# Performance work log

Hardware: AMD Instinct MI355X
Metric: run time of the kernel (lower is better)

Reference implementation:

```python
import jax, jax.numpy as jnp
import numpy as np

SEQ, BZ, DIM = 2048, 16, 1024
NUM_LANG, DICT_LEN = 16, 32000


def setup_inputs() -> dict:
    key = jax.random.key(0)
    ks = jax.random.split(key, 6)
    x = jax.random.normal(ks[0], (SEQ, BZ, DIM), dtype=jnp.float32)
    # raw language ids live at the tail of the dictionary: dict_len-1-raw in [0, num_lang)
    raw = DICT_LEN - 1 - jax.random.randint(ks[1], (BZ,), 0, NUM_LANG)
    W_base = jax.random.normal(ks[2], (DIM, DIM), dtype=jnp.float32) * (DIM ** -0.5)
    b_base = jax.random.normal(ks[3], (DIM,), dtype=jnp.float32) * 0.02
    W = jax.random.uniform(ks[4], (NUM_LANG, DIM, DIM), dtype=jnp.float32) * (DIM ** -0.5)
    bias = jax.random.uniform(ks[5], (NUM_LANG, DIM), dtype=jnp.float32)
    return {"x": x, "lang_ids": raw, "W_base": W_base, "b_base": b_base,
            "W": W, "bias": bias, "dict_len": DICT_LEN, "num_lang": NUM_LANG}


def reference(x, lang_ids, W_base, b_base, W, bias, dict_len, num_lang):
    # Map raw ids to expert indices in [0, num_lang)
    ids = dict_len - 1 - lang_ids                      # [bz]
    # base_model (nn.Linear): h = x @ W_base.T + b_base
    h = jnp.einsum('sbd,ed->sbe', x, W_base) + b_base  # [seq, bz, dim]
    # The original pads each language group to max group size, runs a batched
    # einsum 'abcd,ade->abce' over languages, then scatters back with per-lang
    # bias. Mathematically each batch column j gets W[lang_j] applied:
    We = W[ids]                                        # [bz, dim, dim]
    out = jnp.einsum('sbd,bde->sbe', h, We) + bias[ids][None, :, :]
    return out
```

## Files before the change

kernel.cpp:

```cpp
#include <hip/hip_runtime.h>
#include <stdint.h>

typedef unsigned short u16;
typedef unsigned int u32;
typedef __bf16 bf16x8 __attribute__((ext_vector_type(8)));
typedef float f32x4 __attribute__((ext_vector_type(4)));

#define SEQ 2048
#define BZ 16
#define DIM 1024

__device__ __forceinline__ u16 f2bf(float f) {
    union { float f; u32 u; } a; a.f = f;
    u32 r = a.u + 0x7FFFu + ((a.u >> 16) & 1u);
    return (u16)(r >> 16);
}
__device__ __forceinline__ float bf2f(u16 u) {
    union { u32 u; float f; } a; a.u = ((u32)u) << 16;
    return a.f;
}
__device__ __forceinline__ void async16(const u16* g, u16* l) {
    __builtin_amdgcn_global_load_lds(
        (const __attribute__((address_space(1))) void*)g,
        (__attribute__((address_space(3))) void*)l, 16, 0, 0);
}

__global__ void prep_kernel(const float* __restrict__ x,
                            const float* __restrict__ W,
                            const float* __restrict__ W_base,
                            const int* __restrict__ lang_ids,
                            const int* __restrict__ dict_len,
                            u16* __restrict__ xb,
                            u16* __restrict__ Wt,
                            u16* __restrict__ Wbt)
{
    int bid = blockIdx.x;
    int t = threadIdx.x;
    if (bid < SEQ) {
        int s = bid;
        const float4* src = (const float4*)(x + (size_t)s * BZ * DIM);
        #pragma unroll
        for (int j = 0; j < 16; j++) {
            int idx = j * 256 + t;
            float4 v = src[idx];
            int e = idx * 4;
            int b = e >> 10, d = e & 1023;
            u32 lo = f2bf(v.x) | ((u32)f2bf(v.y) << 16);
            u32 hi = f2bf(v.z) | ((u32)f2bf(v.w) << 16);
            *(uint2*)(xb + ((size_t)b * SEQ + s) * DIM + d) = make_uint2(lo, hi);
        }
        return;
    }
    int tid2 = bid - SEQ;
    int z = tid2 >> 10;
    int yx = tid2 & 1023;
    int by = yx >> 5, bx = yx & 31;
    const float* S;
    u16* D;
    if (z < BZ) {
        int id = dict_len[0] - 1 - lang_ids[z];
        S = W + (size_t)id * DIM * DIM;
        D = Wbt + (size_t)z * DIM * DIM;
    } else {
        S = W_base;
        D = Wt;
    }
    __shared__ float tile[32][33];
    int tx = t & 31, ty = t >> 5;
    int x0 = bx * 32, y0 = by * 32;
    #pragma unroll
    for (int i = 0; i < 4; i++)
        tile[ty + 8 * i][tx] = S[(size_t)(y0 + ty + 8 * i) * DIM + x0 + tx];
    __syncthreads();
    #pragma unroll
    for (int i = 0; i < 4; i++)
        D[(size_t)(x0 + ty + 8 * i) * DIM + y0 + tx] = f2bf(tile[tx][ty + 8 * i]);
}

__global__ void bb_kernel(const u16* __restrict__ Wbt,
                          const float* __restrict__ b_base,
                          const float* __restrict__ bias,
                          const int* __restrict__ lang_ids,
                          const int* __restrict__ dict_len,
                          float* __restrict__ bb)
{
    int gw = blockIdx.x * 4 + (threadIdx.x >> 6);
    int b = gw >> 10;
    int f = gw & 1023;
    int lane = threadIdx.x & 63;
    const u16* row = Wbt + ((size_t)b * DIM + f) * DIM;
    float s = 0.f;
    #pragma unroll
    for (int i = 0; i < DIM / 64; i++)
        s += bf2f(row[lane + 64 * i]) * b_base[lane + 64 * i];
    #pragma unroll
    for (int off = 32; off; off >>= 1)
        s += __shfl_xor(s, off, 64);
    if (lane == 0) {
        int id = dict_len[0] - 1 - lang_ids[b];
        bb[b * DIM + f] = s + bias[(size_t)id * DIM + f];
    }
}


__global__ __launch_bounds__(256, 2)
void gemm1_kernel(const u16* __restrict__ Wbt,
                  const u16* __restrict__ Wt,
                  u16* __restrict__ CT)
{
    int bid = blockIdx.x;
    int virt = ((bid & 7) << 6) + (bid >> 3);
    int b    = virt >> 5;
    int rem  = virt & 31;
    int m0   = (rem >> 2) << 7;
    int n0   = (rem & 3) << 8;

    const u16* A = Wbt + (size_t)b * DIM * DIM;
    const u16* B = Wt;
    u16* C = CT + (size_t)b * DIM * DIM;

    __shared__ u16 As[2 * 128 * 32];
    __shared__ u16 Bs[2 * 256 * 32];

    int tid = threadIdx.x;
    int w = tid >> 6, l = tid & 63;
    int lr = l & 15, quad = l >> 4;

    int srow = l >> 2;
    int chunk = l & 3;
    const u16* gA[2]; const u16* gB[4];
    int lA[2], lB[4];
    #pragma unroll
    for (int j = 0; j < 2; j++) {
        int row = w * 32 + j * 16 + srow;
        gA[j] = A + (size_t)(m0 + row) * DIM + chunk * 8;
        lA[j] = (w * 32 + j * 16) * 32;
    }
    #pragma unroll
    for (int j = 0; j < 4; j++) {
        int row = w * 64 + j * 16 + srow;
        gB[j] = B + (size_t)(n0 + row) * DIM + chunk * 8;
        lB[j] = (w * 64 + j * 16) * 32;
    }

    f32x4 acc[8][4];
    #pragma unroll
    for (int m = 0; m < 8; m++)
        #pragma unroll
        for (int n = 0; n < 4; n++)
            #pragma unroll
            for (int e = 0; e < 4; e++) acc[m][n][e] = 0.f;

    #pragma unroll
    for (int j = 0; j < 2; j++) async16(gA[j], As + lA[j]);
    #pragma unroll
    for (int j = 0; j < 4; j++) async16(gB[j], Bs + lB[j]);
    #pragma unroll
    for (int j = 0; j < 2; j++) gA[j] += 32;
    #pragma unroll
    for (int j = 0; j < 4; j++) gB[j] += 32;
    __syncthreads();

    int cur = 0;
    for (int t = 0; t < DIM / 32; t++) {
        if (t + 1 < DIM / 32) {
            int ao = (cur ^ 1) * 4096, bo = (cur ^ 1) * 8192;
            #pragma unroll
            for (int j = 0; j < 2; j++) { async16(gA[j], As + ao + lA[j]); gA[j] += 32; }
            #pragma unroll
            for (int j = 0; j < 4; j++) { async16(gB[j], Bs + bo + lB[j]); gB[j] += 32; }
        }
        const u16* ra = As + cur * 4096;
        const u16* rb = Bs + cur * 8192;
        bf16x8 af[8], bfv[4];
        #pragma unroll
        for (int m = 0; m < 8; m++)
            af[m] = *(const bf16x8*)&ra[(m * 16 + lr) * 32 + quad * 8];
        #pragma unroll
        for (int n = 0; n < 4; n++)
            bfv[n] = *(const bf16x8*)&rb[(w * 64 + n * 16 + lr) * 32 + quad * 8];
        #pragma unroll
        for (int m = 0; m < 8; m++)
            #pragma unroll
            for (int n = 0; n < 4; n++)
                acc[m][n] = __builtin_amdgcn_mfma_f32_16x16x32_bf16(
                    af[m], bfv[n], acc[m][n], 0, 0, 0);
        __syncthreads();
        cur ^= 1;
    }
    #pragma unroll
    for (int m = 0; m < 8; m++) {
        int fr = m0 + m * 16 + quad * 4;
        #pragma unroll
        for (int n = 0; n < 4; n++) {
            int dc = n0 + w * 64 + n * 16 + lr;
            #pragma unroll
            for (int rr = 0; rr < 4; rr++)
                C[(size_t)(fr + rr) * DIM + dc] = f2bf(acc[m][n][rr]);
        }
    }
}

__global__ __launch_bounds__(256, 2)
void gemm2_kernel(const u16* __restrict__ xb,
                  const u16* __restrict__ CT,
                  const float* __restrict__ bb,
                  float* __restrict__ out)
{
    int bid = blockIdx.x;
    int virt = ((bid & 7) << 7) + (bid >> 3);
    int b    = virt >> 6;
    int rem  = virt & 63;
    int s0   = (rem >> 2) << 7;
    int f0   = (rem & 3) << 8;

    const u16* A  = xb + (size_t)b * SEQ * DIM;
    const u16* Bm = CT + (size_t)b * DIM * DIM;

    __shared__ u16 As[2 * 128 * 32];
    __shared__ u16 Bs[2 * 256 * 32];

    int tid = threadIdx.x;
    int w = tid >> 6, l = tid & 63;
    int lr = l & 15, quad = l >> 4;

    int srow = l >> 2;
    int chunk = l & 3;
    const u16* gA[2]; const u16* gB[4];
    int lA[2], lB[4];
    #pragma unroll
    for (int j = 0; j < 2; j++) {
        int row = w * 32 + j * 16 + srow;
        gA[j] = A + (size_t)(s0 + row) * DIM + chunk * 8;
        lA[j] = (w * 32 + j * 16) * 32;
    }
    #pragma unroll
    for (int j = 0; j < 4; j++) {
        int row = w * 64 + j * 16 + srow;
        gB[j] = Bm + (size_t)(f0 + row) * DIM + chunk * 8;
        lB[j] = (w * 64 + j * 16) * 32;
    }

    f32x4 acc[8][4];
    #pragma unroll
    for (int m = 0; m < 8; m++)
        #pragma unroll
        for (int n = 0; n < 4; n++)
            #pragma unroll
            for (int e = 0; e < 4; e++) acc[m][n][e] = 0.f;

    #pragma unroll
    for (int j = 0; j < 2; j++) async16(gA[j], As + lA[j]);
    #pragma unroll
    for (int j = 0; j < 4; j++) async16(gB[j], Bs + lB[j]);
    #pragma unroll
    for (int j = 0; j < 2; j++) gA[j] += 32;
    #pragma unroll
    for (int j = 0; j < 4; j++) gB[j] += 32;
    __syncthreads();

    int cur = 0;
    for (int t = 0; t < DIM / 32; t++) {
        if (t + 1 < DIM / 32) {
            int ao = (cur ^ 1) * 4096, bo = (cur ^ 1) * 8192;
            #pragma unroll
            for (int j = 0; j < 2; j++) { async16(gA[j], As + ao + lA[j]); gA[j] += 32; }
            #pragma unroll
            for (int j = 0; j < 4; j++) { async16(gB[j], Bs + bo + lB[j]); gB[j] += 32; }
        }
        const u16* ra = As + cur * 4096;
        const u16* rb = Bs + cur * 8192;
        bf16x8 af[8], bfv[4];
        #pragma unroll
        for (int m = 0; m < 8; m++)
            af[m] = *(const bf16x8*)&ra[(m * 16 + lr) * 32 + quad * 8];
        #pragma unroll
        for (int n = 0; n < 4; n++)
            bfv[n] = *(const bf16x8*)&rb[(w * 64 + n * 16 + lr) * 32 + quad * 8];
        #pragma unroll
        for (int m = 0; m < 8; m++)
            #pragma unroll
            for (int n = 0; n < 4; n++)
                acc[m][n] = __builtin_amdgcn_mfma_f32_16x16x32_bf16(
                    af[m], bfv[n], acc[m][n], 0, 0, 0);
        __syncthreads();
        cur ^= 1;
    }

    #pragma unroll
    for (int n = 0; n < 4; n++) {
        int col = f0 + w * 64 + n * 16 + lr;
        float bv = bb[b * DIM + col];
        #pragma unroll
        for (int m = 0; m < 8; m++) {
            int sr = s0 + m * 16 + quad * 4;
            #pragma unroll
            for (int rr = 0; rr < 4; rr++)
                out[((size_t)(sr + rr) * BZ + b) * DIM + col] = acc[m][n][rr] + bv;
        }
    }
}

extern "C" void kernel_launch(void* const* d_in, const int* in_sizes, int n_in,
                              void* d_out, int out_size, void* d_ws, size_t ws_size,
                              hipStream_t stream)
{
    const float* x        = (const float*)d_in[0];
    const int*   lang_ids = (const int*)d_in[1];
    const float* W_base   = (const float*)d_in[2];
    const float* b_base   = (const float*)d_in[3];
    const float* W        = (const float*)d_in[4];
    const float* bias     = (const float*)d_in[5];
    const int*   dict_len = (const int*)d_in[6];
    float* out = (float*)d_out;

    char* ws = (char*)d_ws;
    u16*  Wt  = (u16*)ws;
    u16*  Wbt = (u16*)(ws + (size_t)(2u << 20));
    u16*  CT  = (u16*)(ws + (size_t)(34u << 20));
    float* bb = (float*)(ws + (size_t)(66u << 20));
    u16*  xb  = (u16*)(ws + (size_t)(67u << 20));

    prep_kernel<<<dim3(SEQ + 17 * 1024, 1, 1), 256, 0, stream>>>(
        x, W, W_base, lang_ids, dict_len, xb, Wt, Wbt);
    bb_kernel<<<dim3(4096, 1, 1), 256, 0, stream>>>(
        Wbt, b_base, bias, lang_ids, dict_len, bb);
    gemm1_kernel<<<dim3(512, 1, 1), 256, 0, stream>>>(Wbt, Wt, CT);
    gemm2_kernel<<<dim3(1024, 1, 1), 256, 0, stream>>>(xb, CT, bb, out);
}
```

Baseline: 430.7 us.

## Dedupe per-language weight products and tighten GEMM pipeline barriers

```diff
diff --git a/kernel.cpp b/kernel.cpp
--- a/kernel.cpp
+++ b/kernel.cpp
@@ -10,6 +10,10 @@
 #define BZ 16
 #define DIM 1024
 
+#define WAIT_VM6()   asm volatile("s_waitcnt vmcnt(6)" ::: "memory")
+#define WAIT_VM0()   asm volatile("s_waitcnt vmcnt(0)" ::: "memory")
+#define MEMFENCE()   asm volatile("" ::: "memory")
+
 __device__ __forceinline__ u16 f2bf(float f) {
     union { float f; u32 u; } a; a.f = f;
     u32 r = a.u + 0x7FFFu + ((a.u >> 16) & 1u);
@@ -23,6 +27,13 @@
     __builtin_amdgcn_global_load_lds(
         (const __attribute__((address_space(1))) void*)g,
         (__attribute__((address_space(3))) void*)l, 16, 0, 0);
+}
+__device__ __forceinline__ int rep_of(const int* __restrict__ lang_ids, int b) {
+    int my = lang_ids[b];
+    #pragma unroll
+    for (int j = 0; j < BZ; j++)
+        if (lang_ids[j] == my) return j;
+    return b;
 }
 
 __global__ void prep_kernel(const float* __restrict__ x,
@@ -58,6 +69,7 @@
     const float* S;
     u16* D;
     if (z < BZ) {
+        if (rep_of(lang_ids, z) != z) return;
         int id = dict_len[0] - 1 - lang_ids[z];
         S = W + (size_t)id * DIM * DIM;
         D = Wbt + (size_t)z * DIM * DIM;
@@ -86,6 +98,7 @@
 {
     int gw = blockIdx.x * 4 + (threadIdx.x >> 6);
     int b = gw >> 10;
+    if (rep_of(lang_ids, b) != b) return;
     int f = gw & 1023;
     int lane = threadIdx.x & 63;
     const u16* row = Wbt + ((size_t)b * DIM + f) * DIM;
@@ -106,11 +119,13 @@
 __global__ __launch_bounds__(256, 2)
 void gemm1_kernel(const u16* __restrict__ Wbt,
                   const u16* __restrict__ Wt,
+                  const int* __restrict__ lang_ids,
                   u16* __restrict__ CT)
 {
     int bid = blockIdx.x;
     int virt = ((bid & 7) << 6) + (bid >> 3);
     int b    = virt >> 5;
+    if (rep_of(lang_ids, b) != b) return;
     int rem  = virt & 31;
     int m0   = (rem >> 2) << 7;
     int n0   = (rem & 3) << 8;
@@ -152,24 +167,21 @@
             for (int e = 0; e < 4; e++) acc[m][n][e] = 0.f;
 
     #pragma unroll
-    for (int j = 0; j < 2; j++) async16(gA[j], As + lA[j]);
-    #pragma unroll
-    for (int j = 0; j < 4; j++) async16(gB[j], Bs + lB[j]);
-    #pragma unroll
-    for (int j = 0; j < 2; j++) gA[j] += 32;
-    #pragma unroll
-    for (int j = 0; j < 4; j++) gB[j] += 32;
-    __syncthreads();
+    for (int j = 0; j < 2; j++) { async16(gA[j], As + lA[j]); gA[j] += 32; }
+    #pragma unroll
+    for (int j = 0; j < 4; j++) { async16(gB[j], Bs + lB[j]); gB[j] += 32; }
 
     int cur = 0;
-    for (int t = 0; t < DIM / 32; t++) {
-        if (t + 1 < DIM / 32) {
-            int ao = (cur ^ 1) * 4096, bo = (cur ^ 1) * 8192;
-            #pragma unroll
-            for (int j = 0; j < 2; j++) { async16(gA[j], As + ao + lA[j]); gA[j] += 32; }
-            #pragma unroll
-            for (int j = 0; j < 4; j++) { async16(gB[j], Bs + bo + lB[j]); gB[j] += 32; }
-        }
+    for (int t = 0; t < DIM / 32 - 1; t++) {
+        int ao = (cur ^ 1) * 4096, bo = (cur ^ 1) * 8192;
+        #pragma unroll
+        for (int j = 0; j < 2; j++) { async16(gA[j], As + ao + lA[j]); gA[j] += 32; }
+        #pragma unroll
+        for (int j = 0; j < 4; j++) { async16(gB[j], Bs + bo + lB[j]); gB[j] += 32; }
+        WAIT_VM6();
+        MEMFENCE(); __builtin_amdgcn_s_barrier(); MEMFENCE();
+        __builtin_amdgcn_sched_barrier(0);
+
         const u16* ra = As + cur * 4096;
         const u16* rb = Bs + cur * 8192;
         bf16x8 af[8], bfv[4];
@@ -179,14 +191,37 @@
         #pragma unroll
         for (int n = 0; n < 4; n++)
             bfv[n] = *(const bf16x8*)&rb[(w * 64 + n * 16 + lr) * 32 + quad * 8];
+        __builtin_amdgcn_s_setprio(1);
         #pragma unroll
         for (int m = 0; m < 8; m++)
             #pragma unroll
             for (int n = 0; n < 4; n++)
                 acc[m][n] = __builtin_amdgcn_mfma_f32_16x16x32_bf16(
                     af[m], bfv[n], acc[m][n], 0, 0, 0);
-        __syncthreads();
+        __builtin_amdgcn_s_setprio(0);
+        __builtin_amdgcn_sched_barrier(0);
+        MEMFENCE(); __builtin_amdgcn_s_barrier(); MEMFENCE();
         cur ^= 1;
+    }
+    {
+        WAIT_VM0();
+        MEMFENCE(); __builtin_amdgcn_s_barrier(); MEMFENCE();
+        __builtin_amdgcn_sched_barrier(0);
+        const u16* ra = As + cur * 4096;
+        const u16* rb = Bs + cur * 8192;
+        bf16x8 af[8], bfv[4];
+        #pragma unroll
+        for (int m = 0; m < 8; m++)
+            af[m] = *(const bf16x8*)&ra[(m * 16 + lr) * 32 + quad * 8];
+        #pragma unroll
+        for (int n = 0; n < 4; n++)
+            bfv[n] = *(const bf16x8*)&rb[(w * 64 + n * 16 + lr) * 32 + quad * 8];
+        #pragma unroll
+        for (int m = 0; m < 8; m++)
+            #pragma unroll
+            for (int n = 0; n < 4; n++)
+                acc[m][n] = __builtin_amdgcn_mfma_f32_16x16x32_bf16(
+                    af[m], bfv[n], acc[m][n], 0, 0, 0);
     }
     #pragma unroll
     for (int m = 0; m < 8; m++) {
@@ -205,17 +240,19 @@
 void gemm2_kernel(const u16* __restrict__ xb,
                   const u16* __restrict__ CT,
                   const float* __restrict__ bb,
+                  const int* __restrict__ lang_ids,
                   float* __restrict__ out)
 {
     int bid = blockIdx.x;
     int virt = ((bid & 7) << 7) + (bid >> 3);
     int b    = virt >> 6;
+    int rb_  = rep_of(lang_ids, b);
     int rem  = virt & 63;
     int s0   = (rem >> 2) << 7;
     int f0   = (rem & 3) << 8;
 
     const u16* A  = xb + (size_t)b * SEQ * DIM;
-    const u16* Bm = CT + (size_t)b * DIM * DIM;
+    const u16* Bm = CT + (size_t)rb_ * DIM * DIM;
 
     __shared__ u16 As[2 * 128 * 32];
     __shared__ u16 Bs[2 * 256 * 32];
@@ -250,24 +287,21 @@
             for (int e = 0; e < 4; e++) acc[m][n][e] = 0.f;
 
     #pragma unroll
-    for (int j = 0; j < 2; j++) async16(gA[j], As + lA[j]);
-    #pragma unroll
-    for (int j = 0; j < 4; j++) async16(gB[j], Bs + lB[j]);
-    #pragma unroll
-    for (int j = 0; j < 2; j++) gA[j] += 32;
-    #pragma unroll
-    for (int j = 0; j < 4; j++) gB[j] += 32;
-    __syncthreads();
+    for (int j = 0; j < 2; j++) { async16(gA[j], As + lA[j]); gA[j] += 32; }
+    #pragma unroll
+    for (int j = 0; j < 4; j++) { async16(gB[j], Bs + lB[j]); gB[j] += 32; }
 
     int cur = 0;
-    for (int t = 0; t < DIM / 32; t++) {
-        if (t + 1 < DIM / 32) {
-            int ao = (cur ^ 1) * 4096, bo = (cur ^ 1) * 8192;
-            #pragma unroll
-            for (int j = 0; j < 2; j++) { async16(gA[j], As + ao + lA[j]); gA[j] += 32; }
-            #pragma unroll
-            for (int j = 0; j < 4; j++) { async16(gB[j], Bs + bo + lB[j]); gB[j] += 32; }
-        }
+    for (int t = 0; t < DIM / 32 - 1; t++) {
+        int ao = (cur ^ 1) * 4096, bo = (cur ^ 1) * 8192;
+        #pragma unroll
+        for (int j = 0; j < 2; j++) { async16(gA[j], As + ao + lA[j]); gA[j] += 32; }
+        #pragma unroll
+        for (int j = 0; j < 4; j++) { async16(gB[j], Bs + bo + lB[j]); gB[j] += 32; }
+        WAIT_VM6();
+        MEMFENCE(); __builtin_amdgcn_s_barrier(); MEMFENCE();
+        __builtin_amdgcn_sched_barrier(0);
+
         const u16* ra = As + cur * 4096;
         const u16* rb = Bs + cur * 8192;
         bf16x8 af[8], bfv[4];
@@ -277,20 +311,43 @@
         #pragma unroll
         for (int n = 0; n < 4; n++)
             bfv[n] = *(const bf16x8*)&rb[(w * 64 + n * 16 + lr) * 32 + quad * 8];
+        __builtin_amdgcn_s_setprio(1);
         #pragma unroll
         for (int m = 0; m < 8; m++)
             #pragma unroll
             for (int n = 0; n < 4; n++)
                 acc[m][n] = __builtin_amdgcn_mfma_f32_16x16x32_bf16(
                     af[m], bfv[n], acc[m][n], 0, 0, 0);
-        __syncthreads();
+        __builtin_amdgcn_s_setprio(0);
+        __builtin_amdgcn_sched_barrier(0);
+        MEMFENCE(); __builtin_amdgcn_s_barrier(); MEMFENCE();
         cur ^= 1;
+    }
+    {
+        WAIT_VM0();
+        MEMFENCE(); __builtin_amdgcn_s_barrier(); MEMFENCE();
+        __builtin_amdgcn_sched_barrier(0);
+        const u16* ra = As + cur * 4096;
+        const u16* rb = Bs + cur * 8192;
+        bf16x8 af[8], bfv[4];
+        #pragma unroll
+        for (int m = 0; m < 8; m++)
+            af[m] = *(const bf16x8*)&ra[(m * 16 + lr) * 32 + quad * 8];
+        #pragma unroll
+        for (int n = 0; n < 4; n++)
+            bfv[n] = *(const bf16x8*)&rb[(w * 64 + n * 16 + lr) * 32 + quad * 8];
+        #pragma unroll
+        for (int m = 0; m < 8; m++)
+            #pragma unroll
+            for (int n = 0; n < 4; n++)
+                acc[m][n] = __builtin_amdgcn_mfma_f32_16x16x32_bf16(
+                    af[m], bfv[n], acc[m][n], 0, 0, 0);
     }
 
     #pragma unroll
     for (int n = 0; n < 4; n++) {
         int col = f0 + w * 64 + n * 16 + lr;
-        float bv = bb[b * DIM + col];
+        float bv = bb[rb_ * DIM + col];
         #pragma unroll
         for (int m = 0; m < 8; m++) {
             int sr = s0 + m * 16 + quad * 4;
@@ -325,6 +382,6 @@
         x, W, W_base, lang_ids, dict_len, xb, Wt, Wbt);
     bb_kernel<<<dim3(4096, 1, 1), 256, 0, stream>>>(
         Wbt, b_base, bias, lang_ids, dict_len, bb);
-    gemm1_kernel<<<dim3(512, 1, 1), 256, 0, stream>>>(Wbt, Wt, CT);
-    gemm2_kernel<<<dim3(1024, 1, 1), 256, 0, stream>>>(xb, CT, bb, out);
-}
+    gemm1_kernel<<<dim3(512, 1, 1), 256, 0, stream>>>(Wbt, Wt, lang_ids, CT);
+    gemm2_kernel<<<dim3(1024, 1, 1), 256, 0, stream>>>(xb, CT, bb, lang_ids, out);
+}
```

New measurement: 419.0 us. -2.7%, faster.
